# Optimization experiments

Hardware: AMD Instinct MI355X
Metric: run time of the kernel (lower is better)

Reference implementation:

```python
import jax, jax.numpy as jnp
import numpy as np

N_NODES = 100000
N_EDGES = 1600000
D_IN = 128
D_HID = 128
D_OUT = 64


def setup_inputs() -> dict:
    key = jax.random.key(0)
    ks = jax.random.split(key, 8)
    x = jax.random.normal(ks[0], (N_NODES, D_IN), dtype=jnp.float32)
    edge_index = jax.random.randint(ks[1], (2, N_EDGES), 0, N_NODES, dtype=jnp.int64)
    s1 = 1.0 / np.sqrt(D_IN)
    s2 = 1.0 / np.sqrt(D_HID)
    W1_l = jax.random.normal(ks[2], (D_IN, D_HID), dtype=jnp.float32) * s1
    W1_r = jax.random.normal(ks[3], (D_IN, D_HID), dtype=jnp.float32) * s1
    b1 = jnp.zeros((D_HID,), dtype=jnp.float32)
    W2_l = jax.random.normal(ks[4], (D_HID, D_OUT), dtype=jnp.float32) * s2
    W2_r = jax.random.normal(ks[5], (D_HID, D_OUT), dtype=jnp.float32) * s2
    b2 = jnp.zeros((D_OUT,), dtype=jnp.float32)
    return {"x": x, "edge_index": edge_index, "W1_l": W1_l, "b1": b1,
            "W1_r": W1_r, "W2_l": W2_l, "b2": b2, "W2_r": W2_r}


def _sage_conv(x, src, dst, Wl, bl, Wr, num_nodes):
    # PyG SAGEConv (aggr='mean', root_weight=True):
    #   out = lin_l(mean_{j in N(i)} x_j) + lin_r(x_i)
    agg = jax.ops.segment_sum(x[src], dst, num_segments=num_nodes)        # [N, d]
    deg = jax.ops.segment_sum(jnp.ones((src.shape[0],), dtype=x.dtype), dst,
                              num_segments=num_nodes)                      # [N]
    mean = agg / jnp.maximum(deg, 1.0)[:, None]
    return mean @ Wl + bl + x @ Wr


def reference(x, edge_index, W1_l, b1, W1_r, W2_l, b2, W2_r):
    src, dst = edge_index[0], edge_index[1]
    n = x.shape[0]
    h = jax.nn.relu(_sage_conv(x, src, dst, W1_l, b1, W1_r, n))
    # dropout is identity in eval mode
    out = _sage_conv(h, src, dst, W2_l, b2, W2_r, n)
    return jax.nn.log_softmax(out, axis=1)
```

## Files before the change

kernel.cpp:

```cpp
#include <hip/hip_runtime.h>
#include <math.h>

#define NN 100000
#define NE 1600000
#define SBN 512
#define NSB ((NN + SBN - 1) / SBN)
#define SBCAP 10240
#define EPB 8192
#define NBA ((NE + EPB - 1) / EPB)

typedef __attribute__((ext_vector_type(8))) short bf16x8;
typedef __attribute__((ext_vector_type(8))) unsigned short ush8;
typedef __attribute__((ext_vector_type(4))) float f32x4;

static __device__ __forceinline__ float b2f(unsigned short u) {
    return __uint_as_float(((unsigned int)u) << 16);
}
static __device__ __forceinline__ unsigned short f2bf(float f) {
    unsigned int u = __float_as_uint(f);
    u += 0x7fffu + ((u >> 16) & 1u);
    return (unsigned short)(u >> 16);
}

__global__ __launch_bounds__(256)
void k_cvt_x(const float* __restrict__ in, unsigned short* __restrict__ outb, long total8) {
    long i = (long)blockIdx.x * 256 + threadIdx.x;
    long stride = (long)gridDim.x * 256;
    for (; i < total8; i += stride) {
        const float4* p = (const float4*)(in + i * 8);
        float4 a = p[0], b = p[1];
        ush8 r;
        r[0] = f2bf(a.x); r[1] = f2bf(a.y); r[2] = f2bf(a.z); r[3] = f2bf(a.w);
        r[4] = f2bf(b.x); r[5] = f2bf(b.y); r[6] = f2bf(b.z); r[7] = f2bf(b.w);
        *(ush8*)(outb + i * 8) = r;
    }
}

__global__ __launch_bounds__(256)
void k_cvt_weights(const float* __restrict__ W1l, const float* __restrict__ W1r,
                   const float* __restrict__ W2l, const float* __restrict__ W2r,
                   unsigned short* __restrict__ Wt1l, unsigned short* __restrict__ Wt1r,
                   unsigned short* __restrict__ Wtcat) {
    int id = blockIdx.x * 256 + threadIdx.x;
    int seg = id >> 14;
    int e = id & 16383;
    int n = e >> 7, k = e & 127;
    if (seg == 0)      Wt1l[e] = f2bf(W1l[k * 128 + n]);
    else if (seg == 1) Wt1r[e] = f2bf(W1r[k * 128 + n]);
    else if (seg == 2) {
        float v = (n < 64) ? W2l[k * 64 + n] : W2r[k * 64 + (n - 64)];
        Wtcat[e] = f2bf(v);
    }
}

__global__ __launch_bounds__(1024)
void k_binA(const int* __restrict__ src, const int* __restrict__ dst,
            int* __restrict__ gcnt, int* __restrict__ pairs) {
    __shared__ int lsort[EPB];
    __shared__ int lhist[256];
    __shared__ int lofs[256];
    __shared__ int lpos[NSB];
    __shared__ int gbase[NSB];
    const int tid = threadIdx.x;
    const int base = blockIdx.x * EPB;
    const int cnt = min(EPB, NE - base);

    int v[8], bn[8];
    #pragma unroll
    for (int k = 0; k < 8; ++k) {
        int i = k * 1024 + tid;
        if (i < cnt) {
            int d = dst[base + i], s = src[base + i];
            v[k] = (s << 9) | (d & 511);
            bn[k] = d >> 9;
        } else bn[k] = -1;
    }
    if (tid < 256) lhist[tid] = 0;
    __syncthreads();
    #pragma unroll
    for (int k = 0; k < 8; ++k) if (bn[k] >= 0) atomicAdd(&lhist[bn[k]], 1);
    __syncthreads();
    if (tid < 256) lofs[tid] = lhist[tid];
    __syncthreads();
    for (int d = 1; d < 256; d <<= 1) {
        int u = (tid < 256 && tid >= d) ? lofs[tid - d] : 0;
        __syncthreads();
        if (tid < 256) lofs[tid] += u;
        __syncthreads();
    }
    if (tid < 256) lofs[tid] -= lhist[tid];
    __syncthreads();
    if (tid < NSB) {
        lpos[tid] = lofs[tid];
        gbase[tid] = atomicAdd(&gcnt[tid], lhist[tid]);
    }
    __syncthreads();
    #pragma unroll
    for (int k = 0; k < 8; ++k) if (bn[k] >= 0) {
        int slot = atomicAdd(&lpos[bn[k]], 1);
        lsort[slot] = v[k];
    }
    __syncthreads();
    for (int i = tid; i < cnt; i += 1024) {
        int lo = 0, hi = NSB - 1;
        while (lo < hi) { int mid = (lo + hi + 1) >> 1; if (lofs[mid] <= i) lo = mid; else hi = mid - 1; }
        int off = gbase[lo] + (i - lofs[lo]);
        if (off < SBCAP)
            __builtin_nontemporal_store(lsort[i], &pairs[(size_t)lo * SBCAP + off]);
    }
}

__global__ __launch_bounds__(1024)
void k_sortB(const int* __restrict__ gcnt, int* __restrict__ pairs,
             int* __restrict__ offs, int* __restrict__ deg) {
    __shared__ int lstage[SBCAP];
    __shared__ int lhist[SBN], lscan[SBN], lpos[SBN];
    const int sb = blockIdx.x, tid = threadIdx.x;
    const int cnt = min(gcnt[sb], SBCAP);
    int* __restrict__ region = pairs + (size_t)sb * SBCAP;

    for (int i = tid; i < cnt; i += 1024) lstage[i] = region[i];
    if (tid < SBN) lhist[tid] = 0;
    __syncthreads();
    for (int i = tid; i < cnt; i += 1024) atomicAdd(&lhist[lstage[i] & 511], 1);
    __syncthreads();
    if (tid < SBN) lscan[tid] = lhist[tid];
    __syncthreads();
    for (int d = 1; d < SBN; d <<= 1) {
        int u = (tid < SBN && tid >= d) ? lscan[tid - d] : 0;
        __syncthreads();
        if (tid < SBN) lscan[tid] += u;
        __syncthreads();
    }
    if (tid < SBN) {
        int ex = lscan[tid] - lhist[tid];
        lpos[tid] = ex;
        int node = sb * SBN + tid;
        if (node < NN) { offs[node] = sb * SBCAP + ex; deg[node] = lhist[tid]; }
    }
    __syncthreads();
    for (int i = tid; i < cnt; i += 1024) {
        int val = lstage[i];
        int slot = atomicAdd(&lpos[val & 511], 1);
        region[slot] = val >> 9;
    }
}

__global__ __launch_bounds__(256)
void k_aggregate_bf(const unsigned short* __restrict__ feat, const int* __restrict__ csr,
                    const int* __restrict__ offs, const int* __restrict__ deg,
                    unsigned short* __restrict__ outmean) {
    const int wid = threadIdx.x >> 6, lane = threadIdx.x & 63;
    const int q = lane >> 4, l4 = lane & 15;
    const int node = blockIdx.x * 4 + wid;
    if (node >= NN) return;
    int off = __builtin_amdgcn_readfirstlane(offs[node]);
    int dg  = __builtin_amdgcn_readfirstlane(deg[node]);
    const ush8* __restrict__ f8 = (const ush8*)feat;
    float acc[8];
    #pragma unroll
    for (int i = 0; i < 8; ++i) acc[i] = 0.f;
    int j = 0;
    for (; j + 16 <= dg; j += 16) {
        int e0 = csr[off + j + q];
        int e1 = csr[off + j + 4 + q];
        int e2 = csr[off + j + 8 + q];
        int e3 = csr[off + j + 12 + q];
        ush8 v0 = f8[(size_t)e0 * 16 + l4];
        ush8 v1 = f8[(size_t)e1 * 16 + l4];
        ush8 v2 = f8[(size_t)e2 * 16 + l4];
        ush8 v3 = f8[(size_t)e3 * 16 + l4];
        #pragma unroll
        for (int i = 0; i < 8; ++i)
            acc[i] += (b2f(v0[i]) + b2f(v1[i])) + (b2f(v2[i]) + b2f(v3[i]));
    }
    for (; j + 8 <= dg; j += 8) {
        int e0 = csr[off + j + q];
        int e1 = csr[off + j + 4 + q];
        ush8 v0 = f8[(size_t)e0 * 16 + l4];
        ush8 v1 = f8[(size_t)e1 * 16 + l4];
        #pragma unroll
        for (int i = 0; i < 8; ++i) acc[i] += b2f(v0[i]) + b2f(v1[i]);
    }
    for (; j + 4 <= dg; j += 4) {
        int e0 = csr[off + j + q];
        ush8 v0 = f8[(size_t)e0 * 16 + l4];
        #pragma unroll
        for (int i = 0; i < 8; ++i) acc[i] += b2f(v0[i]);
    }
    int rem = dg - j;
    if (q < rem) {
        int e0 = csr[off + j + q];
        ush8 v0 = f8[(size_t)e0 * 16 + l4];
        #pragma unroll
        for (int i = 0; i < 8; ++i) acc[i] += b2f(v0[i]);
    }
    #pragma unroll
    for (int i = 0; i < 8; ++i) {
        acc[i] += __shfl_xor(acc[i], 16);
        acc[i] += __shfl_xor(acc[i], 32);
    }
    if (q == 0) {
        float inv = 1.0f / (float)(dg > 0 ? dg : 1);
        ush8 r;
        #pragma unroll
        for (int i = 0; i < 8; ++i) r[i] = f2bf(acc[i] * inv);
        ((ush8*)outmean)[(size_t)node * 16 + l4] = r;
    }
}

template <int BN, bool RELU, bool OUTBF>
__global__ __launch_bounds__(256)
void k_gemm_mfma(const unsigned short* __restrict__ Am, const unsigned short* __restrict__ Ax,
                 const unsigned short* __restrict__ Wtl, const unsigned short* __restrict__ Wtr,
                 const float* __restrict__ bias, void* __restrict__ outp) {
    constexpr int BM = 128;
    constexpr int WAVES_N = BN / 64;
    constexpr int WAVES_M = 4 / WAVES_N;
    constexpr int MR = BM / (WAVES_M * 16);
    constexpr int NR = 4;
    __shared__ __align__(16) short As[BM * 40];
    __shared__ __align__(16) short Ws[BN * 40];

    const int tid = threadIdx.x;
    const int wave = tid >> 6, lane = tid & 63;
    const int l15 = lane & 15, kg = lane >> 4;
    const int wc = wave % WAVES_N, wr = wave / WAVES_N;
    const int rowbase = wr * MR * 16;
    const int colbase = wc * 64;
    const int row0 = blockIdx.x * BM;

    f32x4 acc[MR][NR];
    #pragma unroll
    for (int mr = 0; mr < MR; ++mr)
        #pragma unroll
        for (int nr = 0; nr < NR; ++nr) acc[mr][nr] = (f32x4){0.f, 0.f, 0.f, 0.f};

    for (int s = 0; s < 2; ++s) {
        const unsigned short* __restrict__ A  = s ? Ax : Am;
        const unsigned short* __restrict__ Wt = s ? Wtr : Wtl;
        for (int kc = 0; kc < 128; kc += 32) {
            __syncthreads();
            #pragma unroll
            for (int i = 0; i < (BM * 4) / 256; ++i) {
                int c = tid + 256 * i; int r = c >> 2, g = c & 3;
                ush8 v = {0, 0, 0, 0, 0, 0, 0, 0};
                int grow = row0 + r;
                if (grow < NN) v = *(const ush8*)&A[(size_t)grow * 128 + kc + g * 8];
                *(ush8*)&As[r * 40 + g * 8] = v;
            }
            #pragma unroll
            for (int i = 0; i < (BN * 4) / 256; ++i) {
                int c = tid + 256 * i; int n = c >> 2, g = c & 3;
                *(ush8*)&Ws[n * 40 + g * 8] = *(const ush8*)&Wt[n * 128 + kc + g * 8];
            }
            __syncthreads();
            bf16x8 af[MR], bfr[NR];
            #pragma unroll
            for (int mr = 0; mr < MR; ++mr)
                af[mr] = *(const bf16x8*)&As[(rowbase + mr * 16 + l15) * 40 + kg * 8];
            #pragma unroll
            for (int nr = 0; nr < NR; ++nr)
                bfr[nr] = *(const bf16x8*)&Ws[(colbase + nr * 16 + l15) * 40 + kg * 8];
            #pragma unroll
            for (int mr = 0; mr < MR; ++mr)
                #pragma unroll
                for (int nr = 0; nr < NR; ++nr)
                    acc[mr][nr] = __builtin_amdgcn_mfma_f32_16x16x32_bf16(
                        af[mr], bfr[nr], acc[mr][nr], 0, 0, 0);
        }
    }
    const int r4 = kg * 4;
    #pragma unroll
    for (int mr = 0; mr < MR; ++mr) {
        #pragma unroll
        for (int nr = 0; nr < NR; ++nr) {
            int col = colbase + nr * 16 + l15;
            float bv = bias[col];
            #pragma unroll
            for (int j = 0; j < 4; ++j) {
                int row = row0 + rowbase + mr * 16 + r4 + j;
                if (row < NN) {
                    float v = acc[mr][nr][j] + bv;
                    if (RELU) v = fmaxf(v, 0.f);
                    if (OUTBF) ((unsigned short*)outp)[(size_t)row * BN + col] = f2bf(v);
                    else       ((float*)outp)[(size_t)row * BN + col] = v;
                }
            }
        }
    }
}

__global__ __launch_bounds__(256)
void k_gemm_cat(const unsigned short* __restrict__ A, const unsigned short* __restrict__ Wt,
                const float* __restrict__ b2,
                unsigned short* __restrict__ g, unsigned short* __restrict__ z) {
    constexpr int BM = 128, BN = 128, MR = 4, NR = 4;
    __shared__ __align__(16) short As[BM * 40];
    __shared__ __align__(16) short Ws[BN * 40];

    const int tid = threadIdx.x;
    const int wave = tid >> 6, lane = tid & 63;
    const int l15 = lane & 15, kg = lane >> 4;
    const int wc = wave % 2, wr = wave / 2;
    const int rowbase = wr * MR * 16;
    const int colbase = wc * 64;
    const int row0 = blockIdx.x * BM;

    f32x4 acc[MR][NR];
    #pragma unroll
    for (int mr = 0; mr < MR; ++mr)
        #pragma unroll
        for (int nr = 0; nr < NR; ++nr) acc[mr][nr] = (f32x4){0.f, 0.f, 0.f, 0.f};

    for (int kc = 0; kc < 128; kc += 32) {
        __syncthreads();
        #pragma unroll
        for (int i = 0; i < 2; ++i) {
            int c = tid + 256 * i; int r = c >> 2, gg = c & 3;
            ush8 v = {0, 0, 0, 0, 0, 0, 0, 0};
            int grow = row0 + r;
            if (grow < NN) v = *(const ush8*)&A[(size_t)grow * 128 + kc + gg * 8];
            *(ush8*)&As[r * 40 + gg * 8] = v;
        }
        #pragma unroll
        for (int i = 0; i < 2; ++i) {
            int c = tid + 256 * i; int n = c >> 2, gg = c & 3;
            *(ush8*)&Ws[n * 40 + gg * 8] = *(const ush8*)&Wt[n * 128 + kc + gg * 8];
        }
        __syncthreads();
        bf16x8 af[MR], bfr[NR];
        #pragma unroll
        for (int mr = 0; mr < MR; ++mr)
            af[mr] = *(const bf16x8*)&As[(rowbase + mr * 16 + l15) * 40 + kg * 8];
        #pragma unroll
        for (int nr = 0; nr < NR; ++nr)
            bfr[nr] = *(const bf16x8*)&Ws[(colbase + nr * 16 + l15) * 40 + kg * 8];
        #pragma unroll
        for (int mr = 0; mr < MR; ++mr)
            #pragma unroll
            for (int nr = 0; nr < NR; ++nr)
                acc[mr][nr] = __builtin_amdgcn_mfma_f32_16x16x32_bf16(
                    af[mr], bfr[nr], acc[mr][nr], 0, 0, 0);
    }
    const int r4 = kg * 4;
    #pragma unroll
    for (int mr = 0; mr < MR; ++mr) {
        #pragma unroll
        for (int nr = 0; nr < NR; ++nr) {
            int col = colbase + nr * 16 + l15;
            float bv = (col >= 64) ? b2[col - 64] : 0.f;
            #pragma unroll
            for (int j = 0; j < 4; ++j) {
                int row = row0 + rowbase + mr * 16 + r4 + j;
                if (row < NN) {
                    float v = acc[mr][nr][j] + bv;
                    unsigned short bv16 = f2bf(v);
                    if (col < 64) g[(size_t)row * 64 + col] = bv16;
                    else          z[(size_t)row * 64 + (col - 64)] = bv16;
                }
            }
        }
    }
}

__global__ __launch_bounds__(256)
void k_agg_lsm(const unsigned short* __restrict__ gbuf, const unsigned short* __restrict__ zbuf,
               const int* __restrict__ csr, const int* __restrict__ offs,
               const int* __restrict__ deg, float* __restrict__ out) {
    const int wid = threadIdx.x >> 6, lane = threadIdx.x & 63;
    const int g8 = lane >> 3, l8 = lane & 7;
    const int node = blockIdx.x * 4 + wid;
    if (node >= NN) return;
    int off = __builtin_amdgcn_readfirstlane(offs[node]);
    int dg  = __builtin_amdgcn_readfirstlane(deg[node]);
    const ush8* __restrict__ f8 = (const ush8*)gbuf;
    float acc[8];
    #pragma unroll
    for (int i = 0; i < 8; ++i) acc[i] = 0.f;
    int j = 0;
    for (; j + 32 <= dg; j += 32) {
        int e0 = csr[off + j + g8];
        int e1 = csr[off + j + 8 + g8];
        int e2 = csr[off + j + 16 + g8];
        int e3 = csr[off + j + 24 + g8];
        ush8 v0 = f8[(size_t)e0 * 8 + l8];
        ush8 v1 = f8[(size_t)e1 * 8 + l8];
        ush8 v2 = f8[(size_t)e2 * 8 + l8];
        ush8 v3 = f8[(size_t)e3 * 8 + l8];
        #pragma unroll
        for (int i = 0; i < 8; ++i)
            acc[i] += (b2f(v0[i]) + b2f(v1[i])) + (b2f(v2[i]) + b2f(v3[i]));
    }
    for (; j + 16 <= dg; j += 16) {
        int e0 = csr[off + j + g8];
        int e1 = csr[off + j + 8 + g8];
        ush8 v0 = f8[(size_t)e0 * 8 + l8];
        ush8 v1 = f8[(size_t)e1 * 8 + l8];
        #pragma unroll
        for (int i = 0; i < 8; ++i) acc[i] += b2f(v0[i]) + b2f(v1[i]);
    }
    for (; j + 8 <= dg; j += 8) {
        int e0 = csr[off + j + g8];
        ush8 v0 = f8[(size_t)e0 * 8 + l8];
        #pragma unroll
        for (int i = 0; i < 8; ++i) acc[i] += b2f(v0[i]);
    }
    int rem = dg - j;
    if (g8 < rem) {
        int e0 = csr[off + j + g8];
        ush8 v0 = f8[(size_t)e0 * 8 + l8];
        #pragma unroll
        for (int i = 0; i < 8; ++i) acc[i] += b2f(v0[i]);
    }
    #pragma unroll
    for (int i = 0; i < 8; ++i) {
        acc[i] += __shfl_xor(acc[i], 8);
        acc[i] += __shfl_xor(acc[i], 16);
        acc[i] += __shfl_xor(acc[i], 32);
    }
    float inv = 1.0f / (float)(dg > 0 ? dg : 1);
    ush8 zv = ((const ush8*)zbuf)[(size_t)node * 8 + l8];
    float v[8];
    float m = -1e30f;
    #pragma unroll
    for (int i = 0; i < 8; ++i) {
        v[i] = acc[i] * inv + b2f(zv[i]);
        m = fmaxf(m, v[i]);
    }
    #pragma unroll
    for (int d = 4; d >= 1; d >>= 1) m = fmaxf(m, __shfl_xor(m, d));
    float ss = 0.f;
    #pragma unroll
    for (int i = 0; i < 8; ++i) ss += __expf(v[i] - m);
    #pragma unroll
    for (int d = 4; d >= 1; d >>= 1) ss += __shfl_xor(ss, d);
    float lse = m + logf(ss);
    if (g8 == 0) {
        float4 o0 = make_float4(v[0] - lse, v[1] - lse, v[2] - lse, v[3] - lse);
        float4 o1 = make_float4(v[4] - lse, v[5] - lse, v[6] - lse, v[7] - lse);
        *(float4*)&out[(size_t)node * 64 + l8 * 8]     = o0;
        *(float4*)&out[(size_t)node * 64 + l8 * 8 + 4] = o1;
    }
}

extern "C" void kernel_launch(void* const* d_in, const int* in_sizes, int n_in,
                              void* d_out, int out_size, void* d_ws, size_t ws_size,
                              hipStream_t stream) {
    const float* x   = (const float*)d_in[0];
    const int* edges = (const int*)d_in[1];
    const float* W1l = (const float*)d_in[2];
    const float* b1  = (const float*)d_in[3];
    const float* W1r = (const float*)d_in[4];
    const float* W2l = (const float*)d_in[5];
    const float* b2  = (const float*)d_in[6];
    const float* W2r = (const float*)d_in[7];
    float* out = (float*)d_out;

    const int* src = edges;
    const int* dst = edges + NE;

    char* ws = (char*)d_ws;
    size_t o = 0;
    auto alloc = [&](size_t bytes) -> void* {
        void* p = ws + o;
        o = (o + bytes + 255) & ~(size_t)255;
        return p;
    };
    int* gcnt  = (int*)alloc((size_t)NSB * 4);
    int* pairs = (int*)alloc((size_t)NSB * SBCAP * 4);
    int* offs  = (int*)alloc((size_t)NN * 4);
    int* deg   = (int*)alloc((size_t)NN * 4);
    unsigned short* xb    = (unsigned short*)alloc((size_t)NN * 128 * 2);
    unsigned short* meanb = (unsigned short*)alloc((size_t)NN * 128 * 2);
    unsigned short* hb    = (unsigned short*)alloc((size_t)NN * 128 * 2);
    unsigned short* gbuf  = (unsigned short*)alloc((size_t)NN * 64 * 2);
    unsigned short* zbuf  = (unsigned short*)alloc((size_t)NN * 64 * 2);
    unsigned short* Wt1l  = (unsigned short*)alloc(128 * 128 * 2);
    unsigned short* Wt1r  = (unsigned short*)alloc(128 * 128 * 2);
    unsigned short* Wtcat = (unsigned short*)alloc(128 * 128 * 2);

    hipMemsetAsync(gcnt, 0, (size_t)NSB * 4, stream);

    k_cvt_x<<<2048, 256, 0, stream>>>(x, xb, (long)NN * 128 / 8);
    k_cvt_weights<<<(3 * 16384 + 255) / 256, 256, 0, stream>>>(W1l, W1r, W2l, W2r,
                                                               Wt1l, Wt1r, Wtcat);

    k_binA<<<NBA, 1024, 0, stream>>>(src, dst, gcnt, pairs);
    k_sortB<<<NSB, 1024, 0, stream>>>(gcnt, pairs, offs, deg);

    const int GEMM_GRID = (NN + 127) / 128;
    k_aggregate_bf<<<(NN + 3) / 4, 256, 0, stream>>>(xb, pairs, offs, deg, meanb);
    k_gemm_mfma<128, true, true><<<GEMM_GRID, 256, 0, stream>>>(meanb, xb, Wt1l, Wt1r, b1, hb);
    k_gemm_cat<<<GEMM_GRID, 256, 0, stream>>>(hb, Wtcat, b2, gbuf, zbuf);
    k_agg_lsm<<<(NN + 3) / 4, 256, 0, stream>>>(gbuf, zbuf, pairs, offs, deg, out);
}
```

Measured before the change: 219.6 us.

## Fuse layer-1 GEMM and layer-2 concatenated GEMM, keeping hidden tile in LDS

Merges the two GEMM kernels into one. The ReLU hidden activations for each 128-row tile are written as bf16 into shared memory and used directly as the A operand of the second (concatenated W2) GEMM, so the hidden tensor is never written to or read back from global memory. This removes one launch and about 50 MB of HBM traffic. In exchange, the second GEMM reads its weight fragments straight from global or L2 instead of staging them in LDS, and the larger LDS footprint can lower occupancy.

```diff
diff --git a/kernel.cpp b/kernel.cpp
--- a/kernel.cpp
+++ b/kernel.cpp
@@ -209,32 +209,31 @@
     }
 }
 
-template <int BN, bool RELU, bool OUTBF>
 __global__ __launch_bounds__(256)
-void k_gemm_mfma(const unsigned short* __restrict__ Am, const unsigned short* __restrict__ Ax,
-                 const unsigned short* __restrict__ Wtl, const unsigned short* __restrict__ Wtr,
-                 const float* __restrict__ bias, void* __restrict__ outp) {
-    constexpr int BM = 128;
-    constexpr int WAVES_N = BN / 64;
-    constexpr int WAVES_M = 4 / WAVES_N;
-    constexpr int MR = BM / (WAVES_M * 16);
-    constexpr int NR = 4;
-    __shared__ __align__(16) short As[BM * 40];
-    __shared__ __align__(16) short Ws[BN * 40];
+void k_gemm12(const unsigned short* __restrict__ Am, const unsigned short* __restrict__ Ax,
+              const unsigned short* __restrict__ Wtl, const unsigned short* __restrict__ Wtr,
+              const unsigned short* __restrict__ Wtcat,
+              const float* __restrict__ b1, const float* __restrict__ b2,
+              unsigned short* __restrict__ g, unsigned short* __restrict__ z) {
+    __shared__ __align__(16) short lds[17408];
+    short* As = lds;
+    short* Ws = lds + 5120;
+    short* hbL = lds;
 
     const int tid = threadIdx.x;
     const int wave = tid >> 6, lane = tid & 63;
     const int l15 = lane & 15, kg = lane >> 4;
-    const int wc = wave % WAVES_N, wr = wave / WAVES_N;
-    const int rowbase = wr * MR * 16;
+    const int wc = wave & 1, wr = wave >> 1;
+    const int rowbase = wr * 64;
     const int colbase = wc * 64;
-    const int row0 = blockIdx.x * BM;
-
-    f32x4 acc[MR][NR];
-    #pragma unroll
-    for (int mr = 0; mr < MR; ++mr)
-        #pragma unroll
-        for (int nr = 0; nr < NR; ++nr) acc[mr][nr] = (f32x4){0.f, 0.f, 0.f, 0.f};
+    const int row0 = blockIdx.x * 128;
+    const int r4 = kg * 4;
+
+    f32x4 acc[4][4];
+    #pragma unroll
+    for (int mr = 0; mr < 4; ++mr)
+        #pragma unroll
+        for (int nr = 0; nr < 4; ++nr) acc[mr][nr] = (f32x4){0.f, 0.f, 0.f, 0.f};
 
     for (int s = 0; s < 2; ++s) {
         const unsigned short* __restrict__ A  = s ? Ax : Am;
@@ -242,112 +241,76 @@
         for (int kc = 0; kc < 128; kc += 32) {
             __syncthreads();
             #pragma unroll
-            for (int i = 0; i < (BM * 4) / 256; ++i) {
-                int c = tid + 256 * i; int r = c >> 2, g = c & 3;
+            for (int i = 0; i < 2; ++i) {
+                int c = tid + 256 * i; int r = c >> 2, gq = c & 3;
                 ush8 v = {0, 0, 0, 0, 0, 0, 0, 0};
                 int grow = row0 + r;
-                if (grow < NN) v = *(const ush8*)&A[(size_t)grow * 128 + kc + g * 8];
-                *(ush8*)&As[r * 40 + g * 8] = v;
+                if (grow < NN) v = *(const ush8*)&A[(size_t)grow * 128 + kc + gq * 8];
+                *(ush8*)&As[r * 40 + gq * 8] = v;
             }
             #pragma unroll
-            for (int i = 0; i < (BN * 4) / 256; ++i) {
-                int c = tid + 256 * i; int n = c >> 2, g = c & 3;
-                *(ush8*)&Ws[n * 40 + g * 8] = *(const ush8*)&Wt[n * 128 + kc + g * 8];
+            for (int i = 0; i < 2; ++i) {
+                int c = tid + 256 * i; int n = c >> 2, gq = c & 3;
+                *(ush8*)&Ws[n * 40 + gq * 8] = *(const ush8*)&Wt[n * 128 + kc + gq * 8];
             }
             __syncthreads();
-            bf16x8 af[MR], bfr[NR];
-            #pragma unroll
-            for (int mr = 0; mr < MR; ++mr)
+            bf16x8 af[4], bfr[4];
+            #pragma unroll
+            for (int mr = 0; mr < 4; ++mr)
                 af[mr] = *(const bf16x8*)&As[(rowbase + mr * 16 + l15) * 40 + kg * 8];
             #pragma unroll
-            for (int nr = 0; nr < NR; ++nr)
+            for (int nr = 0; nr < 4; ++nr)
                 bfr[nr] = *(const bf16x8*)&Ws[(colbase + nr * 16 + l15) * 40 + kg * 8];
             #pragma unroll
-            for (int mr = 0; mr < MR; ++mr)
+            for (int mr = 0; mr < 4; ++mr)
                 #pragma unroll
-                for (int nr = 0; nr < NR; ++nr)
+                for (int nr = 0; nr < 4; ++nr)
                     acc[mr][nr] = __builtin_amdgcn_mfma_f32_16x16x32_bf16(
                         af[mr], bfr[nr], acc[mr][nr], 0, 0, 0);
         }
     }
-    const int r4 = kg * 4;
-    #pragma unroll
-    for (int mr = 0; mr < MR; ++mr) {
-        #pragma unroll
-        for (int nr = 0; nr < NR; ++nr) {
-            int col = colbase + nr * 16 + l15;
-            float bv = bias[col];
+
+    __syncthreads();
+    #pragma unroll
+    for (int nr = 0; nr < 4; ++nr) {
+        int col = colbase + nr * 16 + l15;
+        float bv = b1[col];
+        #pragma unroll
+        for (int mr = 0; mr < 4; ++mr) {
             #pragma unroll
             for (int j = 0; j < 4; ++j) {
-                int row = row0 + rowbase + mr * 16 + r4 + j;
-                if (row < NN) {
-                    float v = acc[mr][nr][j] + bv;
-                    if (RELU) v = fmaxf(v, 0.f);
-                    if (OUTBF) ((unsigned short*)outp)[(size_t)row * BN + col] = f2bf(v);
-                    else       ((float*)outp)[(size_t)row * BN + col] = v;
-                }
+                int rl = rowbase + mr * 16 + r4 + j;
+                float v = fmaxf(acc[mr][nr][j] + bv, 0.f);
+                hbL[rl * 136 + col] = (short)f2bf(v);
             }
         }
     }
-}
-
-__global__ __launch_bounds__(256)
-void k_gemm_cat(const unsigned short* __restrict__ A, const unsigned short* __restrict__ Wt,
-                const float* __restrict__ b2,
-                unsigned short* __restrict__ g, unsigned short* __restrict__ z) {
-    constexpr int BM = 128, BN = 128, MR = 4, NR = 4;
-    __shared__ __align__(16) short As[BM * 40];
-    __shared__ __align__(16) short Ws[BN * 40];
-
-    const int tid = threadIdx.x;
-    const int wave = tid >> 6, lane = tid & 63;
-    const int l15 = lane & 15, kg = lane >> 4;
-    const int wc = wave % 2, wr = wave / 2;
-    const int rowbase = wr * MR * 16;
-    const int colbase = wc * 64;
-    const int row0 = blockIdx.x * BM;
-
-    f32x4 acc[MR][NR];
-    #pragma unroll
-    for (int mr = 0; mr < MR; ++mr)
-        #pragma unroll
-        for (int nr = 0; nr < NR; ++nr) acc[mr][nr] = (f32x4){0.f, 0.f, 0.f, 0.f};
-
+    __syncthreads();
+
+    #pragma unroll
+    for (int mr = 0; mr < 4; ++mr)
+        #pragma unroll
+        for (int nr = 0; nr < 4; ++nr) acc[mr][nr] = (f32x4){0.f, 0.f, 0.f, 0.f};
+    #pragma unroll
     for (int kc = 0; kc < 128; kc += 32) {
-        __syncthreads();
-        #pragma unroll
-        for (int i = 0; i < 2; ++i) {
-            int c = tid + 256 * i; int r = c >> 2, gg = c & 3;
-            ush8 v = {0, 0, 0, 0, 0, 0, 0, 0};
-            int grow = row0 + r;
-            if (grow < NN) v = *(const ush8*)&A[(size_t)grow * 128 + kc + gg * 8];
-            *(ush8*)&As[r * 40 + gg * 8] = v;
-        }
-        #pragma unroll
-        for (int i = 0; i < 2; ++i) {
-            int c = tid + 256 * i; int n = c >> 2, gg = c & 3;
-            *(ush8*)&Ws[n * 40 + gg * 8] = *(const ush8*)&Wt[n * 128 + kc + gg * 8];
-        }
-        __syncthreads();
-        bf16x8 af[MR], bfr[NR];
-        #pragma unroll
-        for (int mr = 0; mr < MR; ++mr)
-            af[mr] = *(const bf16x8*)&As[(rowbase + mr * 16 + l15) * 40 + kg * 8];
-        #pragma unroll
-        for (int nr = 0; nr < NR; ++nr)
-            bfr[nr] = *(const bf16x8*)&Ws[(colbase + nr * 16 + l15) * 40 + kg * 8];
-        #pragma unroll
-        for (int mr = 0; mr < MR; ++mr)
-            #pragma unroll
-            for (int nr = 0; nr < NR; ++nr)
+        bf16x8 af[4], bfr[4];
+        #pragma unroll
+        for (int mr = 0; mr < 4; ++mr)
+            af[mr] = *(const bf16x8*)&hbL[(rowbase + mr * 16 + l15) * 136 + kc + kg * 8];
+        #pragma unroll
+        for (int nr = 0; nr < 4; ++nr)
+            bfr[nr] = *(const bf16x8*)&Wtcat[(size_t)(colbase + nr * 16 + l15) * 128 + kc + kg * 8];
+        #pragma unroll
+        for (int mr = 0; mr < 4; ++mr)
+            #pragma unroll
+            for (int nr = 0; nr < 4; ++nr)
                 acc[mr][nr] = __builtin_amdgcn_mfma_f32_16x16x32_bf16(
                     af[mr], bfr[nr], acc[mr][nr], 0, 0, 0);
     }
-    const int r4 = kg * 4;
-    #pragma unroll
-    for (int mr = 0; mr < MR; ++mr) {
-        #pragma unroll
-        for (int nr = 0; nr < NR; ++nr) {
+    #pragma unroll
+    for (int mr = 0; mr < 4; ++mr) {
+        #pragma unroll
+        for (int nr = 0; nr < 4; ++nr) {
             int col = colbase + nr * 16 + l15;
             float bv = (col >= 64) ? b2[col - 64] : 0.f;
             #pragma unroll
@@ -473,7 +436,6 @@
     int* deg   = (int*)alloc((size_t)NN * 4);
     unsigned short* xb    = (unsigned short*)alloc((size_t)NN * 128 * 2);
     unsigned short* meanb = (unsigned short*)alloc((size_t)NN * 128 * 2);
-    unsigned short* hb    = (unsigned short*)alloc((size_t)NN * 128 * 2);
     unsigned short* gbuf  = (unsigned short*)alloc((size_t)NN * 64 * 2);
     unsigned short* zbuf  = (unsigned short*)alloc((size_t)NN * 64 * 2);
     unsigned short* Wt1l  = (unsigned short*)alloc(128 * 128 * 2);
@@ -491,7 +453,6 @@
 
     const int GEMM_GRID = (NN + 127) / 128;
     k_aggregate_bf<<<(NN + 3) / 4, 256, 0, stream>>>(xb, pairs, offs, deg, meanb);
-    k_gemm_mfma<128, true, true><<<GEMM_GRID, 256, 0, stream>>>(meanb, xb, Wt1l, Wt1r, b1, hb);
-    k_gemm_cat<<<GEMM_GRID, 256, 0, stream>>>(hb, Wtcat, b2, gbuf, zbuf);
+    k_gemm12<<<GEMM_GRID, 256, 0, stream>>>(meanb, xb, Wt1l, Wt1r, Wtcat, b1, b2, gbuf, zbuf);
     k_agg_lsm<<<(NN + 3) / 4, 256, 0, stream>>>(gbuf, zbuf, pairs, offs, deg, out);
 }
```

Result: faster. 205.4 us (-6.5%).
